# Optimization experiments

Measured on AMD Instinct MI355X. Metric: run time of the kernel, lower is better.

The kernel has to match this reference:

```python
import jax, jax.numpy as jnp
import numpy as np

STEPS = 250
BETA = 0.02


def setup_inputs() -> dict:
    key = jax.random.key(0)
    k1, k2 = jax.random.split(key)
    reflectance_normal = jax.random.normal(k1, (8, 1024, 1024), dtype=jnp.float32)
    distribution = jax.random.normal(k2, (8, 65536), dtype=jnp.float32)
    return {"reflectance_normal": reflectance_normal, "distribution": distribution}


def reference(reflectance_normal, distribution):
    # Faithful vectorized version of ForwardDiffusionModel.forward:
    # per batch element, 250 steps of xt = sqrt(1-b)*xt + sqrt(b)*sample,
    # where sample is drawn i.i.d. uniformly (with replacement) from the
    # flattened empirical distribution values of that batch element.
    B = reflectance_normal.shape[0]
    flat = distribution.reshape(B, -1)          # [B, N]
    N = flat.shape[1]
    a = np.sqrt(1.0 - BETA).astype(np.float32)
    b = np.sqrt(BETA).astype(np.float32)
    sample_shape = reflectance_normal.shape     # [B, H, W]

    keys = jax.random.split(jax.random.key(42), STEPS)

    def step(xt, k):
        idx = jax.random.randint(k, sample_shape, 0, N)                 # [B,H,W]
        sample = jnp.take_along_axis(flat, idx.reshape(B, -1), axis=1)  # [B,H*W]
        sample = sample.reshape(sample_shape)
        return a * xt + b * sample, None

    xt, _ = jax.lax.scan(step, reflectance_normal, keys)
    return xt
```

## Files before the change

### kernel.cpp

```cpp
#include <hip/hip_runtime.h>
#include <hip/hip_fp16.h>
#include <stdint.h>

#define WG 512
#define G 8
#define NDIST 65536
#define NLDS 31744
#define NSTEPS 250

#define TF_ROUND(r) { x0 += x1; x1 = (x1 << (r)) | (x1 >> (32 - (r))); x1 ^= x0; }

__device__ __forceinline__ uint2 threefry2x32(uint32_t ks0, uint32_t ks1, uint32_t ks2,
                                              uint32_t x0, uint32_t x1) {
  x0 += ks0; x1 += ks1;
  TF_ROUND(13) TF_ROUND(15) TF_ROUND(26) TF_ROUND(6)
  x0 += ks1; x1 += ks2 + 1u;
  TF_ROUND(17) TF_ROUND(29) TF_ROUND(16) TF_ROUND(24)
  x0 += ks2; x1 += ks0 + 2u;
  TF_ROUND(13) TF_ROUND(15) TF_ROUND(26) TF_ROUND(6)
  x0 += ks0; x1 += ks1 + 3u;
  TF_ROUND(17) TF_ROUND(29) TF_ROUND(16) TF_ROUND(24)
  x0 += ks1; x1 += ks2 + 4u;
  TF_ROUND(13) TF_ROUND(15) TF_ROUND(26) TF_ROUND(6)
  x0 += ks2; x1 += ks0 + 5u;
  return make_uint2(x0, x1);
}

__global__ __launch_bounds__(WG, 1) void fwd_diff_hyb(
    const float* __restrict__ x_init,
    const float* __restrict__ dist,
    float* __restrict__ out) {
  __shared__ __half   tab[NLDS];
  __shared__ uint32_t keys[2 * NSTEPS];

  const int tid   = threadIdx.x;
  const int batch = blockIdx.x >> 8;
  const int chunk = blockIdx.x & 255;
  const uint32_t base = ((uint32_t)batch << 20) + ((uint32_t)chunk << 12);

  const float Ac = 0.9899494936611665f;
  const float Bc = 0.1414213562373095f;

  const float* __restrict__ row = dist + (size_t)batch * NDIST;

  const float4* src4 = reinterpret_cast<const float4*>(row);
  for (int i = tid; i < NLDS / 4; i += WG) {
    float4 v = src4[i];
    ushort4 h;
    h.x = __half_as_ushort(__float2half(Bc * v.x));
    h.y = __half_as_ushort(__float2half(Bc * v.y));
    h.z = __half_as_ushort(__float2half(Bc * v.z));
    h.w = __half_as_ushort(__float2half(Bc * v.w));
    *reinterpret_cast<ushort4*>(&tab[i * 4]) = h;
  }

  if (tid < NSTEPS) {
    uint2 ks = threefry2x32(0u, 42u, 0x1BD11BDAu ^ 42u, 0u, (uint32_t)tid);
    uint2 k2 = threefry2x32(ks.x, ks.y, ks.x ^ ks.y ^ 0x1BD11BDAu, 0u, 1u);
    keys[2 * tid]     = k2.x;
    keys[2 * tid + 1] = k2.y;
  }
  __syncthreads();

  uint32_t p[G];
  float acc[G];
#pragma unroll
  for (int j = 0; j < G; ++j) {
    p[j]   = base + (uint32_t)(j * WG) + (uint32_t)tid;
    acc[j] = x_init[p[j]];
  }

  for (int s = 0; s < NSTEPS; ++s) {
    uint32_t kx = keys[2 * s];
    uint32_t ky = keys[2 * s + 1];
    kx = (uint32_t)__builtin_amdgcn_readfirstlane((int)kx);
    ky = (uint32_t)__builtin_amdgcn_readfirstlane((int)ky);
    const uint32_t kz = kx ^ ky ^ 0x1BD11BDAu;
#pragma unroll
    for (int j = 0; j < G; ++j) {
      uint2 r = threefry2x32(kx, ky, kz, 0u, p[j]);
      uint32_t idx = r.y & 0xFFFFu;
      float sv;
      if (idx < NLDS) {
        sv = __half2float(tab[idx]);
      } else {
        sv = Bc * row[idx];
      }
      acc[j] = fmaf(Ac, acc[j], sv);
    }
  }

#pragma unroll
  for (int j = 0; j < G; ++j) out[p[j]] = acc[j];
}

extern "C" void kernel_launch(void* const* d_in, const int* in_sizes, int n_in,
                              void* d_out, int out_size, void* d_ws, size_t ws_size,
                              hipStream_t stream) {
  const float* x_init = (const float*)d_in[0];
  const float* dist   = (const float*)d_in[1];
  if (n_in >= 2 && in_sizes[0] == 8 * NDIST) {
    x_init = (const float*)d_in[1];
    dist   = (const float*)d_in[0];
  }
  float* out = (float*)d_out;

  fwd_diff_hyb<<<dim3(2048), dim3(WG), 0, stream>>>(x_init, dist, out);
}
```

Baseline: 4.115 ms.

## Hold full fp16 distribution table in LDS with larger workgroups

Adds a kernel that stores the entire 65536-entry scaled distribution as fp16 in 128 KB of dynamic LDS, so every gathered sample comes from LDS. This removes the divergent global-memory fallback for indices beyond the old partial table. Workgroups grow to 1024 threads and each processes 8192 elements. The host checks dynamic-LDS support and occupancy and falls back to the old hybrid kernel if the check fails.

```diff
diff --git a/kernel.cpp b/kernel.cpp
--- a/kernel.cpp
+++ b/kernel.cpp
@@ -2,10 +2,7 @@
 #include <hip/hip_fp16.h>
 #include <stdint.h>
 
-#define WG 512
-#define G 8
 #define NDIST 65536
-#define NLDS 31744
 #define NSTEPS 250
 
 #define TF_ROUND(r) { x0 += x1; x1 = (x1 << (r)) | (x1 >> (32 - (r))); x1 ^= x0; }
@@ -26,7 +23,78 @@
   return make_uint2(x0, x1);
 }
 
-__global__ __launch_bounds__(WG, 1) void fwd_diff_hyb(
+__device__ __forceinline__ void init_keys(uint32_t* keys, int tid) {
+  if (tid < NSTEPS) {
+    uint2 ks = threefry2x32(0u, 42u, 0x1BD11BDAu ^ 42u, 0u, (uint32_t)tid);
+    uint2 k2 = threefry2x32(ks.x, ks.y, ks.x ^ ks.y ^ 0x1BD11BDAu, 0u, 1u);
+    keys[2 * tid]     = k2.x;
+    keys[2 * tid + 1] = k2.y;
+  }
+}
+
+#define WGL 1024
+#define GL  8
+
+__global__ __launch_bounds__(WGL, 1) void fwd_diff_full(
+    const float* __restrict__ x_init,
+    const float* __restrict__ dist,
+    float* __restrict__ out) {
+  extern __shared__ char smem[];
+  __half*   tab  = reinterpret_cast<__half*>(smem);
+  uint32_t* keys = reinterpret_cast<uint32_t*>(smem + 131072);
+
+  const int tid   = threadIdx.x;
+  const int batch = blockIdx.x >> 7;
+  const int chunk = blockIdx.x & 127;
+  const uint32_t base = ((uint32_t)batch << 20) + ((uint32_t)chunk << 13);
+
+  const float Ac = 0.9899494936611665f;
+  const float Bc = 0.1414213562373095f;
+
+  const float4* src = reinterpret_cast<const float4*>(dist + (size_t)batch * NDIST);
+  for (int i = tid; i < NDIST / 4; i += WGL) {
+    float4 v = src[i];
+    ushort4 h;
+    h.x = __half_as_ushort(__float2half(Bc * v.x));
+    h.y = __half_as_ushort(__float2half(Bc * v.y));
+    h.z = __half_as_ushort(__float2half(Bc * v.z));
+    h.w = __half_as_ushort(__float2half(Bc * v.w));
+    reinterpret_cast<ushort4*>(tab)[i] = h;
+  }
+  init_keys(keys, tid);
+  __syncthreads();
+
+  uint32_t p[GL];
+  float acc[GL];
+#pragma unroll
+  for (int j = 0; j < GL; ++j) {
+    p[j]   = base + (uint32_t)(j * WGL) + (uint32_t)tid;
+    acc[j] = x_init[p[j]];
+  }
+
+  for (int s = 0; s < NSTEPS; ++s) {
+    uint32_t kx = keys[2 * s];
+    uint32_t ky = keys[2 * s + 1];
+    kx = (uint32_t)__builtin_amdgcn_readfirstlane((int)kx);
+    ky = (uint32_t)__builtin_amdgcn_readfirstlane((int)ky);
+    const uint32_t kz = kx ^ ky ^ 0x1BD11BDAu;
+#pragma unroll
+    for (int j = 0; j < GL; ++j) {
+      uint2 r = threefry2x32(kx, ky, kz, 0u, p[j]);
+      uint32_t idx = r.y & 0xFFFFu;
+      acc[j] = fmaf(Ac, acc[j], __half2float(tab[idx]));
+    }
+  }
+
+#pragma unroll
+  for (int j = 0; j < GL; ++j) out[p[j]] = acc[j];
+}
+
+#define WGH 512
+#define GH  8
+#define NLDS 31744
+
+__global__ __launch_bounds__(WGH, 1) void fwd_diff_hyb(
     const float* __restrict__ x_init,
     const float* __restrict__ dist,
     float* __restrict__ out) {
@@ -44,7 +112,7 @@
   const float* __restrict__ row = dist + (size_t)batch * NDIST;
 
   const float4* src4 = reinterpret_cast<const float4*>(row);
-  for (int i = tid; i < NLDS / 4; i += WG) {
+  for (int i = tid; i < NLDS / 4; i += WGH) {
     float4 v = src4[i];
     ushort4 h;
     h.x = __half_as_ushort(__float2half(Bc * v.x));
@@ -53,20 +121,14 @@
     h.w = __half_as_ushort(__float2half(Bc * v.w));
     *reinterpret_cast<ushort4*>(&tab[i * 4]) = h;
   }
-
-  if (tid < NSTEPS) {
-    uint2 ks = threefry2x32(0u, 42u, 0x1BD11BDAu ^ 42u, 0u, (uint32_t)tid);
-    uint2 k2 = threefry2x32(ks.x, ks.y, ks.x ^ ks.y ^ 0x1BD11BDAu, 0u, 1u);
-    keys[2 * tid]     = k2.x;
-    keys[2 * tid + 1] = k2.y;
-  }
+  init_keys(keys, tid);
   __syncthreads();
 
-  uint32_t p[G];
-  float acc[G];
+  uint32_t p[GH];
+  float acc[GH];
 #pragma unroll
-  for (int j = 0; j < G; ++j) {
-    p[j]   = base + (uint32_t)(j * WG) + (uint32_t)tid;
+  for (int j = 0; j < GH; ++j) {
+    p[j]   = base + (uint32_t)(j * WGH) + (uint32_t)tid;
     acc[j] = x_init[p[j]];
   }
 
@@ -77,21 +139,18 @@
     ky = (uint32_t)__builtin_amdgcn_readfirstlane((int)ky);
     const uint32_t kz = kx ^ ky ^ 0x1BD11BDAu;
 #pragma unroll
-    for (int j = 0; j < G; ++j) {
+    for (int j = 0; j < GH; ++j) {
       uint2 r = threefry2x32(kx, ky, kz, 0u, p[j]);
       uint32_t idx = r.y & 0xFFFFu;
       float sv;
-      if (idx < NLDS) {
-        sv = __half2float(tab[idx]);
-      } else {
-        sv = Bc * row[idx];
-      }
+      if (idx < NLDS) sv = __half2float(tab[idx]);
+      else            sv = Bc * row[idx];
       acc[j] = fmaf(Ac, acc[j], sv);
     }
   }
 
 #pragma unroll
-  for (int j = 0; j < G; ++j) out[p[j]] = acc[j];
+  for (int j = 0; j < GH; ++j) out[p[j]] = acc[j];
 }
 
 extern "C" void kernel_launch(void* const* d_in, const int* in_sizes, int n_in,
@@ -105,5 +164,20 @@
   }
   float* out = (float*)d_out;
 
-  fwd_diff_hyb<<<dim3(2048), dim3(WG), 0, stream>>>(x_init, dist, out);
+  const int smem_bytes = 131072 + 2048;
+
+  hipError_t st = hipFuncSetAttribute(
+      reinterpret_cast<const void*>(fwd_diff_full),
+      hipFuncAttributeMaxDynamicSharedMemorySize, smem_bytes);
+  int max_blocks = 0;
+  if (st == hipSuccess) {
+    st = hipOccupancyMaxActiveBlocksPerMultiprocessor(
+        &max_blocks, reinterpret_cast<const void*>(fwd_diff_full), WGL, smem_bytes);
+  }
+
+  if (st == hipSuccess && max_blocks >= 1) {
+    fwd_diff_full<<<dim3(1024), dim3(WGL), smem_bytes, stream>>>(x_init, dist, out);
+  } else {
+    fwd_diff_hyb<<<dim3(2048), dim3(WGH), 0, stream>>>(x_init, dist, out);
+  }
 }
```

Result: faster. 3.556 ms (-13.6%).
